# Kernel optimization log

Measured on AMD Instinct MI355X. Metric: run time of the kernel, lower is better.

Reference implementation:

```python
import jax, jax.numpy as jnp
import numpy as np

B, S, DM = 4, 8192, 1024
N_RED = 16384   # tokens merged into their right neighbor
N_SAVE = 16384  # tokens kept; must be divisible by B


def setup_inputs() -> dict:
    key = jax.random.key(0)
    k1, k2, k3, k4 = jax.random.split(key, 4)
    x = jax.random.normal(k1, (B, S, DM), dtype=jnp.float32)
    W = jax.random.normal(k2, (DM, DM), dtype=jnp.float32) * (1.0 / np.sqrt(DM))
    ids_to_reduce = jax.random.randint(k3, (N_RED,), 0, B * S - 1, dtype=jnp.int64)
    ids_to_save = jax.random.randint(k4, (N_SAVE,), 0, B * S, dtype=jnp.int64)
    return {"x": x, "W": W, "ids_to_save": ids_to_save, "ids_to_reduce": ids_to_reduce}


def reference(x, W, ids_to_save, ids_to_reduce):
    batch_size, _, dm = x.shape
    xf = x.reshape(-1, dm)                       # [B*S, dm]
    reduced = xf[ids_to_reduce]                  # gather  [N_RED, dm]
    transformed = (reduced @ W.T).astype(jnp.float32)  # Linear, no bias
    xf = xf.at[ids_to_reduce + 1].add(transformed)     # scatter-add into right neighbor
    saved = xf[ids_to_save]                      # gather  [N_SAVE, dm]
    return saved.reshape(batch_size, -1, dm)     # [B, N_SAVE//B, dm]
```

## Files before the change

kernel.cpp:

```cpp
#include <hip/hip_runtime.h>

#define DM    1024
#define NTOK  32768
#define NRED  16384
#define NSAVE 16384
#define MMAX  16384

typedef __attribute__((ext_vector_type(8))) short bf16x8;
typedef __attribute__((ext_vector_type(4))) float f32x4;

__device__ __forceinline__ ushort f2bf(float f) {
    union { float f; unsigned u; } v; v.f = f;
    unsigned r = (v.u + 0x7FFF + ((v.u >> 16) & 1)) >> 16;
    return (ushort)r;
}
__device__ __forceinline__ float bf2f(ushort u) {
    union { unsigned u; float f; } v; v.u = ((unsigned)u) << 16;
    return v.f;
}

__global__ __launch_bounds__(256) void setup_kernel(const float* __restrict__ W,
                                                    ushort* __restrict__ Wb,
                                                    int* __restrict__ cnt,
                                                    int* __restrict__ need,
                                                    int* __restrict__ counter) {
    int t = blockIdx.x * 256 + threadIdx.x;
    float4 v = ((const float4*)W)[t];
    ushort4 o;
    o.x = f2bf(v.x); o.y = f2bf(v.y); o.z = f2bf(v.z); o.w = f2bf(v.w);
    ((ushort4*)Wb)[t] = o;
    if (t < NTOK) { cnt[t] = 0; need[t] = 0; }
    if (t == 0) *counter = 0;
}

__global__ __launch_bounds__(256) void prep_kernel(const int* __restrict__ red,
                                                   const int* __restrict__ sav,
                                                   int* __restrict__ cnt,
                                                   int* __restrict__ need) {
    int j = blockIdx.x * 256 + threadIdx.x;
    if (j >= NRED) return;
    atomicAdd(&cnt[red[j]], 1);
    int s = sav[j];
    if (s > 0) need[s - 1] = 1;
}

__global__ __launch_bounds__(256) void compact_kernel(const int* __restrict__ cnt,
                                                      const int* __restrict__ need,
                                                      int* __restrict__ inv,
                                                      int* __restrict__ list,
                                                      int* __restrict__ counter) {
    int t = blockIdx.x * 256 + threadIdx.x;
    if (t >= NTOK) return;
    if (need[t] && cnt[t] > 0) {
        int pos = atomicAdd(counter, 1);
        inv[t] = pos;
        list[pos] = t;
    }
}

__global__ __launch_bounds__(256) void convx_kernel(const float* __restrict__ X,
                                                    const int* __restrict__ list,
                                                    const int* __restrict__ counter,
                                                    ushort* __restrict__ Xb) {
    const int M = *counter;
    const int Mpad = (M + 127) & ~127;
    for (int r = blockIdx.x; r < Mpad; r += gridDim.x) {
        ushort4 o;
        if (r < M) {
            int src = list[r];
            float4 v = ((const float4*)(X + (size_t)src * DM))[threadIdx.x];
            o.x = f2bf(v.x); o.y = f2bf(v.y); o.z = f2bf(v.z); o.w = f2bf(v.w);
        } else {
            o.x = 0; o.y = 0; o.z = 0; o.w = 0;
        }
        ((ushort4*)(Xb + (size_t)r * DM))[threadIdx.x] = o;
    }
}

__global__ __launch_bounds__(256) void gemm_kernel(const ushort* __restrict__ Xb,
                                                   const ushort* __restrict__ Wb,
                                                   const int* __restrict__ counter,
                                                   ushort* __restrict__ Tb) {
    const int M = *counter;
    const int m0 = blockIdx.x * 128;
    if (m0 >= M) return;
    const int n0 = blockIdx.y * 128;

    __shared__ char lds[65536];

    const int tid  = threadIdx.x;
    const int l    = tid & 63;
    const int w    = tid >> 6;

    const int srow   = l >> 3;
    const int schunk = (l & 7) ^ (srow & 7);
    const ushort* aS = Xb + (size_t)(m0 + w * 32 + srow) * DM + schunk * 8;
    const ushort* bS = Wb + (size_t)(n0 + w * 32 + srow) * DM + schunk * 8;
    const int dOff   = (w * 32) * 128;

#define STAGE(buf, k0) do {                                                          \
    char* _a = lds + (buf) * 32768 + dOff;                                           \
    _Pragma("unroll")                                                                \
    for (int _i = 0; _i < 4; ++_i) {                                                 \
        __builtin_amdgcn_global_load_lds(                                            \
            (const __attribute__((address_space(1))) unsigned*)(aS + (k0) + _i * 8 * DM), \
            (__attribute__((address_space(3))) unsigned*)(_a + _i * 1024), 16, 0, 0);      \
        __builtin_amdgcn_global_load_lds(                                            \
            (const __attribute__((address_space(1))) unsigned*)(bS + (k0) + _i * 8 * DM), \
            (__attribute__((address_space(3))) unsigned*)(_a + 16384 + _i * 1024), 16, 0, 0); \
    }                                                                                \
} while (0)

    const int kgrp = l >> 4;
    const int r16  = l & 15;
    int aoff[2][2], boff[8][2];
#pragma unroll
    for (int fm = 0; fm < 2; ++fm) {
        int row = w * 32 + fm * 16 + r16;
#pragma unroll
        for (int kk = 0; kk < 2; ++kk)
            aoff[fm][kk] = row * 128 + (((kk * 4 + kgrp) ^ (row & 7)) * 16);
    }
#pragma unroll
    for (int fn = 0; fn < 8; ++fn) {
        int row = fn * 16 + r16;
#pragma unroll
        for (int kk = 0; kk < 2; ++kk)
            boff[fn][kk] = 16384 + row * 128 + (((kk * 4 + kgrp) ^ (row & 7)) * 16);
    }

    f32x4 acc[2][8] = {};

    STAGE(0, 0);
#pragma unroll
    for (int t = 0; t < 16; ++t) {
        const char* base = lds + (t & 1) * 32768;
        if (t < 15) {
            STAGE((t & 1) ^ 1, (t + 1) * 64);
            asm volatile("s_waitcnt vmcnt(8)" ::: "memory");
        } else {
            asm volatile("s_waitcnt vmcnt(0)" ::: "memory");
        }
        __builtin_amdgcn_sched_barrier(0);
        __builtin_amdgcn_s_barrier();

#pragma unroll
        for (int kk = 0; kk < 2; ++kk) {
            bf16x8 af[2], bfr[8];
#pragma unroll
            for (int fm = 0; fm < 2; ++fm) af[fm]  = *(const bf16x8*)(base + aoff[fm][kk]);
#pragma unroll
            for (int fn = 0; fn < 8; ++fn) bfr[fn] = *(const bf16x8*)(base + boff[fn][kk]);
#pragma unroll
            for (int fm = 0; fm < 2; ++fm)
#pragma unroll
                for (int fn = 0; fn < 8; ++fn)
                    acc[fm][fn] = __builtin_amdgcn_mfma_f32_16x16x32_bf16(af[fm], bfr[fn], acc[fm][fn], 0, 0, 0);
        }

        if (t < 15)
            __builtin_amdgcn_s_barrier();
    }
#undef STAGE

#pragma unroll
    for (int fm = 0; fm < 2; ++fm) {
        int mbase = m0 + w * 32 + fm * 16 + kgrp * 4;
#pragma unroll
        for (int fn = 0; fn < 8; ++fn) {
            int n = n0 + fn * 16 + r16;
#pragma unroll
            for (int r = 0; r < 4; ++r) {
                int m = mbase + r;
                if (m < M) Tb[(size_t)m * DM + n] = f2bf(acc[fm][fn][r]);
            }
        }
    }
}

__global__ __launch_bounds__(256) void out_kernel(const float* __restrict__ X,
                                                  const ushort* __restrict__ Tb,
                                                  const int* __restrict__ sav,
                                                  const int* __restrict__ cnt,
                                                  const int* __restrict__ inv,
                                                  float* __restrict__ out) {
    int r = blockIdx.x;
    int d = threadIdx.x;
    int s = sav[r];
    const float4* xr = (const float4*)(X + (size_t)s * DM);
    float4 v = xr[d];
    if (s > 0) {
        int t = s - 1;
        int c = cnt[t];
        if (c > 0) {
            float fc = (float)c;
            const ushort4* tr = (const ushort4*)(Tb + (size_t)inv[t] * DM);
            ushort4 wv = tr[d];
            v.x += fc * bf2f(wv.x); v.y += fc * bf2f(wv.y);
            v.z += fc * bf2f(wv.z); v.w += fc * bf2f(wv.w);
        }
    }
    ((float4*)out)[(size_t)r * (DM / 4) + d] = v;
}

extern "C" void kernel_launch(void* const* d_in, const int* in_sizes, int n_in,
                              void* d_out, int out_size, void* d_ws, size_t ws_size,
                              hipStream_t stream) {
    const float* X   = (const float*)d_in[0];
    const float* W   = (const float*)d_in[1];
    const int*   sav = (const int*)d_in[2];
    const int*   red = (const int*)d_in[3];
    float* out = (float*)d_out;

    char* ws = (char*)d_ws;
    int* counter = (int*)ws;
    int* cnt  = counter + 64;
    int* need = cnt + NTOK;
    int* inv  = need + NTOK;
    int* list = inv + NTOK;
    ushort* Wb = (ushort*)(ws + (1 << 19));
    ushort* Xb = (ushort*)(ws + (4 << 20));
    ushort* Tb = (ushort*)(ws + (36u << 20));

    setup_kernel<<<DM * DM / 4 / 256, 256, 0, stream>>>(W, Wb, cnt, need, counter);
    prep_kernel<<<NRED / 256, 256, 0, stream>>>(red, sav, cnt, need);
    compact_kernel<<<NTOK / 256, 256, 0, stream>>>(cnt, need, inv, list, counter);
    convx_kernel<<<2048, 256, 0, stream>>>(X, list, counter, Xb);

    dim3 ggrid(MMAX / 128, DM / 128);
    gemm_kernel<<<ggrid, 256, 0, stream>>>(Xb, Wb, counter, Tb);

    out_kernel<<<NSAVE, 256, 0, stream>>>(X, Tb, sav, cnt, inv, out);
}
```

Baseline: 67.34 us.

## Switch GEMM to 32x32x16 MFMA with two waves per 128x128 tile

The GEMM kernel now issues 32x32x16 bf16 MFMAs instead of 16x16x32, and the 128x128 tile is computed by 2 waves of 64x128 each instead of 4 waves of 32x128. Each wave loads twice as many rows per stage and keeps 8 accumulators of 16 floats. The aim is fewer LDS fragment reads per FLOP and higher MFMA density per instruction. The cost is more accumulator registers per wave and fewer waves per block to hide latency, and the output store pattern is remapped to match the 32x32 accumulator layout.

```diff
diff --git a/kernel.cpp b/kernel.cpp
--- a/kernel.cpp
+++ b/kernel.cpp
@@ -6,8 +6,9 @@
 #define NSAVE 16384
 #define MMAX  16384
 
-typedef __attribute__((ext_vector_type(8))) short bf16x8;
-typedef __attribute__((ext_vector_type(4))) float f32x4;
+typedef __attribute__((ext_vector_type(8)))  short bf16x8;
+typedef __attribute__((ext_vector_type(4)))  float f32x4;
+typedef __attribute__((ext_vector_type(16))) float f32x16;
 
 __device__ __forceinline__ ushort f2bf(float f) {
     union { float f; unsigned u; } v; v.f = f;
@@ -77,7 +78,7 @@
     }
 }
 
-__global__ __launch_bounds__(256) void gemm_kernel(const ushort* __restrict__ Xb,
+__global__ __launch_bounds__(128) void gemm_kernel(const ushort* __restrict__ Xb,
                                                    const ushort* __restrict__ Wb,
                                                    const int* __restrict__ counter,
                                                    ushort* __restrict__ Tb) {
@@ -88,48 +89,38 @@
 
     __shared__ char lds[65536];
 
-    const int tid  = threadIdx.x;
-    const int l    = tid & 63;
-    const int w    = tid >> 6;
+    const int tid = threadIdx.x;
+    const int l   = tid & 63;
+    const int w   = tid >> 6;
 
     const int srow   = l >> 3;
     const int schunk = (l & 7) ^ (srow & 7);
-    const ushort* aS = Xb + (size_t)(m0 + w * 32 + srow) * DM + schunk * 8;
-    const ushort* bS = Wb + (size_t)(n0 + w * 32 + srow) * DM + schunk * 8;
-    const int dOff   = (w * 32) * 128;
+    const ushort* aS = Xb + (size_t)(m0 + w * 64 + srow) * DM + schunk * 8;
+    const ushort* bS = Wb + (size_t)(n0 + w * 64 + srow) * DM + schunk * 8;
 
 #define STAGE(buf, k0) do {                                                          \
-    char* _a = lds + (buf) * 32768 + dOff;                                           \
+    char* _d = lds + (buf) * 32768 + w * 8192;                                       \
     _Pragma("unroll")                                                                \
-    for (int _i = 0; _i < 4; ++_i) {                                                 \
+    for (int _i = 0; _i < 8; ++_i) {                                                 \
         __builtin_amdgcn_global_load_lds(                                            \
             (const __attribute__((address_space(1))) unsigned*)(aS + (k0) + _i * 8 * DM), \
-            (__attribute__((address_space(3))) unsigned*)(_a + _i * 1024), 16, 0, 0);      \
+            (__attribute__((address_space(3))) unsigned*)(_d + _i * 1024), 16, 0, 0);      \
         __builtin_amdgcn_global_load_lds(                                            \
             (const __attribute__((address_space(1))) unsigned*)(bS + (k0) + _i * 8 * DM), \
-            (__attribute__((address_space(3))) unsigned*)(_a + 16384 + _i * 1024), 16, 0, 0); \
+            (__attribute__((address_space(3))) unsigned*)(_d + 16384 + _i * 1024), 16, 0, 0); \
     }                                                                                \
 } while (0)
 
-    const int kgrp = l >> 4;
-    const int r16  = l & 15;
-    int aoff[2][2], boff[8][2];
-#pragma unroll
-    for (int fm = 0; fm < 2; ++fm) {
-        int row = w * 32 + fm * 16 + r16;
-#pragma unroll
-        for (int kk = 0; kk < 2; ++kk)
-            aoff[fm][kk] = row * 128 + (((kk * 4 + kgrp) ^ (row & 7)) * 16);
-    }
-#pragma unroll
-    for (int fn = 0; fn < 8; ++fn) {
-        int row = fn * 16 + r16;
-#pragma unroll
-        for (int kk = 0; kk < 2; ++kk)
-            boff[fn][kk] = 16384 + row * 128 + (((kk * 4 + kgrp) ^ (row & 7)) * 16);
-    }
-
-    f32x4 acc[2][8] = {};
+    const int h  = l >> 5;
+    const int e  = l & 7;
+    const int r32 = l & 31;
+    int arow[2], brow[4];
+#pragma unroll
+    for (int fm = 0; fm < 2; ++fm) arow[fm] = (w * 64 + fm * 32 + r32) * 128;
+#pragma unroll
+    for (int fn = 0; fn < 4; ++fn) brow[fn] = 16384 + (fn * 32 + r32) * 128;
+
+    f32x16 acc[2][4] = {};
 
     STAGE(0, 0);
 #pragma unroll
@@ -137,7 +128,7 @@
         const char* base = lds + (t & 1) * 32768;
         if (t < 15) {
             STAGE((t & 1) ^ 1, (t + 1) * 64);
-            asm volatile("s_waitcnt vmcnt(8)" ::: "memory");
+            asm volatile("s_waitcnt vmcnt(16)" ::: "memory");
         } else {
             asm volatile("s_waitcnt vmcnt(0)" ::: "memory");
         }
@@ -145,17 +136,18 @@
         __builtin_amdgcn_s_barrier();
 
 #pragma unroll
-        for (int kk = 0; kk < 2; ++kk) {
-            bf16x8 af[2], bfr[8];
-#pragma unroll
-            for (int fm = 0; fm < 2; ++fm) af[fm]  = *(const bf16x8*)(base + aoff[fm][kk]);
-#pragma unroll
-            for (int fn = 0; fn < 8; ++fn) bfr[fn] = *(const bf16x8*)(base + boff[fn][kk]);
+        for (int ks = 0; ks < 4; ++ks) {
+            const int cs = (((ks * 2 + h) ^ e) << 4);
+            bf16x8 af[2], bfr[4];
+#pragma unroll
+            for (int fm = 0; fm < 2; ++fm) af[fm]  = *(const bf16x8*)(base + arow[fm] + cs);
+#pragma unroll
+            for (int fn = 0; fn < 4; ++fn) bfr[fn] = *(const bf16x8*)(base + brow[fn] + cs);
 #pragma unroll
             for (int fm = 0; fm < 2; ++fm)
 #pragma unroll
-                for (int fn = 0; fn < 8; ++fn)
-                    acc[fm][fn] = __builtin_amdgcn_mfma_f32_16x16x32_bf16(af[fm], bfr[fn], acc[fm][fn], 0, 0, 0);
+                for (int fn = 0; fn < 4; ++fn)
+                    acc[fm][fn] = __builtin_amdgcn_mfma_f32_32x32x16_bf16(af[fm], bfr[fn], acc[fm][fn], 0, 0, 0);
         }
 
         if (t < 15)
@@ -165,13 +157,13 @@
 
 #pragma unroll
     for (int fm = 0; fm < 2; ++fm) {
-        int mbase = m0 + w * 32 + fm * 16 + kgrp * 4;
-#pragma unroll
-        for (int fn = 0; fn < 8; ++fn) {
-            int n = n0 + fn * 16 + r16;
-#pragma unroll
-            for (int r = 0; r < 4; ++r) {
-                int m = mbase + r;
+        int mband = m0 + w * 64 + fm * 32;
+#pragma unroll
+        for (int fn = 0; fn < 4; ++fn) {
+            int n = n0 + fn * 32 + r32;
+#pragma unroll
+            for (int r = 0; r < 16; ++r) {
+                int m = mband + (r & 3) + 8 * (r >> 2) + 4 * h;
                 if (m < M) Tb[(size_t)m * DM + n] = f2bf(acc[fm][fn][r]);
             }
         }
@@ -228,7 +220,7 @@
     convx_kernel<<<2048, 256, 0, stream>>>(X, list, counter, Xb);
 
     dim3 ggrid(MMAX / 128, DM / 128);
-    gemm_kernel<<<ggrid, 256, 0, stream>>>(Xb, Wb, counter, Tb);
+    gemm_kernel<<<ggrid, 128, 0, stream>>>(Xb, Wb, counter, Tb);
 
     out_kernel<<<NSAVE, 256, 0, stream>>>(X, Tb, sav, cnt, inv, out);
 }
```

Result: slower. 69.63 us (+3.4%).

## Switch GEMM to triple-buffered K=32 stages with MFMA priority boost

Applied to the files above, without the earlier changes.

The GEMM main loop moves from double-buffered 64-wide K stages to triple-buffered 32-wide K stages over 48KB of LDS, keeping two stages of loads in flight ahead of compute. The XOR swizzle on LDS is dropped in favour of a plain 64-byte row layout, and s_setprio is raised around the MFMA block. The goal is to hide global-to-LDS latency better and raise occupancy by using less LDS. In exchange it runs twice as many barriers per tile and may add LDS bank conflicts now that the swizzle is gone.

```diff
diff --git a/kernel.cpp b/kernel.cpp
--- a/kernel.cpp
+++ b/kernel.cpp
@@ -86,79 +86,77 @@
     if (m0 >= M) return;
     const int n0 = blockIdx.y * 128;
 
-    __shared__ char lds[65536];
-
-    const int tid  = threadIdx.x;
-    const int l    = tid & 63;
-    const int w    = tid >> 6;
-
-    const int srow   = l >> 3;
-    const int schunk = (l & 7) ^ (srow & 7);
-    const ushort* aS = Xb + (size_t)(m0 + w * 32 + srow) * DM + schunk * 8;
-    const ushort* bS = Wb + (size_t)(n0 + w * 32 + srow) * DM + schunk * 8;
-    const int dOff   = (w * 32) * 128;
-
-#define STAGE(buf, k0) do {                                                          \
-    char* _a = lds + (buf) * 32768 + dOff;                                           \
-    _Pragma("unroll")                                                                \
-    for (int _i = 0; _i < 4; ++_i) {                                                 \
-        __builtin_amdgcn_global_load_lds(                                            \
-            (const __attribute__((address_space(1))) unsigned*)(aS + (k0) + _i * 8 * DM), \
-            (__attribute__((address_space(3))) unsigned*)(_a + _i * 1024), 16, 0, 0);      \
-        __builtin_amdgcn_global_load_lds(                                            \
-            (const __attribute__((address_space(1))) unsigned*)(bS + (k0) + _i * 8 * DM), \
-            (__attribute__((address_space(3))) unsigned*)(_a + 16384 + _i * 1024), 16, 0, 0); \
-    }                                                                                \
+    __shared__ char lds[49152];
+
+    const int tid = threadIdx.x;
+    const int l   = tid & 63;
+    const int w   = tid >> 6;
+
+    const int srow = l >> 2;
+    const int sc   = l & 3;
+    const ushort* aS = Xb + (size_t)(m0 + w * 32 + srow) * DM + sc * 8;
+    const ushort* bS = Wb + (size_t)(n0 + w * 32 + srow) * DM + sc * 8;
+    const int dOff = w * 2048;
+
+#define STAGE(buf, kstep) do {                                                        \
+    char* _d = lds + (buf) * 16384 + dOff;                                            \
+    const int _k = (kstep) * 32;                                                      \
+    __builtin_amdgcn_global_load_lds(                                                 \
+        (const __attribute__((address_space(1))) unsigned*)(aS + _k),                 \
+        (__attribute__((address_space(3))) unsigned*)(_d), 16, 0, 0);                 \
+    __builtin_amdgcn_global_load_lds(                                                 \
+        (const __attribute__((address_space(1))) unsigned*)(aS + _k + 16 * DM),       \
+        (__attribute__((address_space(3))) unsigned*)(_d + 1024), 16, 0, 0);          \
+    __builtin_amdgcn_global_load_lds(                                                 \
+        (const __attribute__((address_space(1))) unsigned*)(bS + _k),                 \
+        (__attribute__((address_space(3))) unsigned*)(_d + 8192), 16, 0, 0);          \
+    __builtin_amdgcn_global_load_lds(                                                 \
+        (const __attribute__((address_space(1))) unsigned*)(bS + _k + 16 * DM),       \
+        (__attribute__((address_space(3))) unsigned*)(_d + 8192 + 1024), 16, 0, 0);   \
 } while (0)
 
     const int kgrp = l >> 4;
     const int r16  = l & 15;
-    int aoff[2][2], boff[8][2];
-#pragma unroll
-    for (int fm = 0; fm < 2; ++fm) {
-        int row = w * 32 + fm * 16 + r16;
-#pragma unroll
-        for (int kk = 0; kk < 2; ++kk)
-            aoff[fm][kk] = row * 128 + (((kk * 4 + kgrp) ^ (row & 7)) * 16);
-    }
-#pragma unroll
-    for (int fn = 0; fn < 8; ++fn) {
-        int row = fn * 16 + r16;
-#pragma unroll
-        for (int kk = 0; kk < 2; ++kk)
-            boff[fn][kk] = 16384 + row * 128 + (((kk * 4 + kgrp) ^ (row & 7)) * 16);
-    }
+    int aoff[2], boff[8];
+#pragma unroll
+    for (int fm = 0; fm < 2; ++fm)
+        aoff[fm] = (w * 32 + fm * 16 + r16) * 64 + kgrp * 16;
+#pragma unroll
+    for (int fn = 0; fn < 8; ++fn)
+        boff[fn] = 8192 + (fn * 16 + r16) * 64 + kgrp * 16;
 
     f32x4 acc[2][8] = {};
 
     STAGE(0, 0);
-#pragma unroll
-    for (int t = 0; t < 16; ++t) {
-        const char* base = lds + (t & 1) * 32768;
-        if (t < 15) {
-            STAGE((t & 1) ^ 1, (t + 1) * 64);
+    STAGE(1, 1);
+#pragma unroll
+    for (int t = 0; t < 32; ++t) {
+        const char* base = lds + (t % 3) * 16384;
+        if (t < 30) {
+            STAGE((t + 2) % 3, t + 2);
             asm volatile("s_waitcnt vmcnt(8)" ::: "memory");
+        } else if (t == 30) {
+            asm volatile("s_waitcnt vmcnt(4)" ::: "memory");
         } else {
             asm volatile("s_waitcnt vmcnt(0)" ::: "memory");
         }
         __builtin_amdgcn_sched_barrier(0);
         __builtin_amdgcn_s_barrier();
 
-#pragma unroll
-        for (int kk = 0; kk < 2; ++kk) {
-            bf16x8 af[2], bfr[8];
-#pragma unroll
-            for (int fm = 0; fm < 2; ++fm) af[fm]  = *(const bf16x8*)(base + aoff[fm][kk]);
-#pragma unroll
-            for (int fn = 0; fn < 8; ++fn) bfr[fn] = *(const bf16x8*)(base + boff[fn][kk]);
-#pragma unroll
-            for (int fm = 0; fm < 2; ++fm)
-#pragma unroll
-                for (int fn = 0; fn < 8; ++fn)
-                    acc[fm][fn] = __builtin_amdgcn_mfma_f32_16x16x32_bf16(af[fm], bfr[fn], acc[fm][fn], 0, 0, 0);
-        }
-
-        if (t < 15)
+        bf16x8 af[2], bfr[8];
+#pragma unroll
+        for (int fm = 0; fm < 2; ++fm) af[fm]  = *(const bf16x8*)(base + aoff[fm]);
+#pragma unroll
+        for (int fn = 0; fn < 8; ++fn) bfr[fn] = *(const bf16x8*)(base + boff[fn]);
+        __builtin_amdgcn_s_setprio(1);
+#pragma unroll
+        for (int fm = 0; fm < 2; ++fm)
+#pragma unroll
+            for (int fn = 0; fn < 8; ++fn)
+                acc[fm][fn] = __builtin_amdgcn_mfma_f32_16x16x32_bf16(af[fm], bfr[fn], acc[fm][fn], 0, 0, 0);
+        __builtin_amdgcn_s_setprio(0);
+
+        if (t < 31)
             __builtin_amdgcn_s_barrier();
     }
 #undef STAGE
```

After: 77.08 us (median of 3 runs). 1.14x slower.

## Use idle GEMM blocks to copy unmodified saved rows, split output kernel

Applied to the files above, without the earlier changes.

The GEMM grid is sized for the maximum row count, so blocks beyond the actual M used to exit immediately. Those idle blocks now copy saved rows that need no added transform straight from X to the output, which overlaps that copy with the GEMM. The output kernel now handles only rows that depend on the GEMM result. The cost is extra reads of sav and cnt in both kernels, plus load imbalance that depends on how many GEMM blocks are idle.

```diff
diff --git a/kernel.cpp b/kernel.cpp
--- a/kernel.cpp
+++ b/kernel.cpp
@@ -80,23 +80,40 @@
 __global__ __launch_bounds__(256) void gemm_kernel(const ushort* __restrict__ Xb,
                                                    const ushort* __restrict__ Wb,
                                                    const int* __restrict__ counter,
-                                                   ushort* __restrict__ Tb) {
+                                                   ushort* __restrict__ Tb,
+                                                   const float* __restrict__ X,
+                                                   const int* __restrict__ sav,
+                                                   const int* __restrict__ cnt,
+                                                   float* __restrict__ out) {
     const int M = *counter;
     const int m0 = blockIdx.x * 128;
-    if (m0 >= M) return;
+    const int tid = threadIdx.x;
+
+    if (m0 >= M) {
+        const int nAct  = (M + 127) >> 7;
+        const int idleId = (blockIdx.x - nAct) * gridDim.y + blockIdx.y;
+        const int nIdle  = (gridDim.x - nAct) * gridDim.y;
+        for (int r = idleId; r < NSAVE; r += nIdle) {
+            int s = sav[r];
+            if (s > 0 && cnt[s - 1] > 0) continue;
+            ((float4*)out)[(size_t)r * 256 + tid] =
+                ((const float4*)(X + (size_t)s * DM))[tid];
+        }
+        return;
+    }
+
     const int n0 = blockIdx.y * 128;
 
     __shared__ char lds[65536];
 
-    const int tid  = threadIdx.x;
-    const int l    = tid & 63;
-    const int w    = tid >> 6;
+    const int l = tid & 63;
+    const int w = tid >> 6;
 
     const int srow   = l >> 3;
     const int schunk = (l & 7) ^ (srow & 7);
     const ushort* aS = Xb + (size_t)(m0 + w * 32 + srow) * DM + schunk * 8;
     const ushort* bS = Wb + (size_t)(n0 + w * 32 + srow) * DM + schunk * 8;
-    const int dOff   = (w * 32) * 128;
+    const int dOff = w * 4096;
 
 #define STAGE(buf, k0) do {                                                          \
     char* _a = lds + (buf) * 32768 + dOff;                                           \
@@ -178,29 +195,24 @@
     }
 }
 
-__global__ __launch_bounds__(256) void out_kernel(const float* __restrict__ X,
-                                                  const ushort* __restrict__ Tb,
-                                                  const int* __restrict__ sav,
-                                                  const int* __restrict__ cnt,
-                                                  const int* __restrict__ inv,
-                                                  float* __restrict__ out) {
+__global__ __launch_bounds__(256) void out_dep_kernel(const float* __restrict__ X,
+                                                      const ushort* __restrict__ Tb,
+                                                      const int* __restrict__ sav,
+                                                      const int* __restrict__ cnt,
+                                                      const int* __restrict__ inv,
+                                                      float* __restrict__ out) {
     int r = blockIdx.x;
+    int s = sav[r];
+    if (s == 0) return;
+    int c = cnt[s - 1];
+    if (c == 0) return;
     int d = threadIdx.x;
-    int s = sav[r];
-    const float4* xr = (const float4*)(X + (size_t)s * DM);
-    float4 v = xr[d];
-    if (s > 0) {
-        int t = s - 1;
-        int c = cnt[t];
-        if (c > 0) {
-            float fc = (float)c;
-            const ushort4* tr = (const ushort4*)(Tb + (size_t)inv[t] * DM);
-            ushort4 wv = tr[d];
-            v.x += fc * bf2f(wv.x); v.y += fc * bf2f(wv.y);
-            v.z += fc * bf2f(wv.z); v.w += fc * bf2f(wv.w);
-        }
-    }
-    ((float4*)out)[(size_t)r * (DM / 4) + d] = v;
+    float fc = (float)c;
+    float4 v = ((const float4*)(X + (size_t)s * DM))[d];
+    ushort4 wv = ((const ushort4*)(Tb + (size_t)inv[s - 1] * DM))[d];
+    v.x += fc * bf2f(wv.x); v.y += fc * bf2f(wv.y);
+    v.z += fc * bf2f(wv.z); v.w += fc * bf2f(wv.w);
+    ((float4*)out)[(size_t)r * 256 + d] = v;
 }
 
 extern "C" void kernel_launch(void* const* d_in, const int* in_sizes, int n_in,
@@ -228,7 +240,7 @@
     convx_kernel<<<2048, 256, 0, stream>>>(X, list, counter, Xb);
 
     dim3 ggrid(MMAX / 128, DM / 128);
-    gemm_kernel<<<ggrid, 256, 0, stream>>>(Xb, Wb, counter, Tb);
-
-    out_kernel<<<NSAVE, 256, 0, stream>>>(X, Tb, sav, cnt, inv, out);
-}
+    gemm_kernel<<<ggrid, 256, 0, stream>>>(Xb, Wb, counter, Tb, X, sav, cnt, out);
+
+    out_dep_kernel<<<NSAVE, 256, 0, stream>>>(X, Tb, sav, cnt, inv, out);
+}
```

Result: slower. 71.14 us (+5.7%).
